# Kernel optimization log

Measured on AMD Instinct MI355X. Metric: run time of the kernel, lower is better.

## Reference

```python
import jax, jax.numpy as jnp
import numpy as np

N_NODES = 100000
N_EDGES = 3200000
N_GRAPHS = 64
NEG_SLOPE = 0.2


def mish(x):
    return x * jnp.tanh(jax.nn.softplus(x))


def gat_layer(x, src, dst, W, b, a_src, a_dst, heads, out_ch, n_nodes):
    # h: [N, H, C]
    h = (x @ W).reshape(n_nodes, heads, out_ch)
    alpha_s = jnp.sum(h * a_src[None], axis=-1)  # [N, H]
    alpha_d = jnp.sum(h * a_dst[None], axis=-1)  # [N, H]
    e = jax.nn.leaky_relu(alpha_s[src] + alpha_d[dst], NEG_SLOPE)  # [E, H]
    # scatter-softmax over incoming edges of each destination node
    emax = jax.ops.segment_max(e, dst, num_segments=n_nodes)  # [N, H]
    ee = jnp.exp(e - emax[dst])
    den = jax.ops.segment_sum(ee, dst, num_segments=n_nodes)
    alpha = ee / (den[dst] + 1e-16)  # [E, H]
    msg = h[src] * alpha[..., None]  # [E, H, C]
    out = jax.ops.segment_sum(msg, dst, num_segments=n_nodes)
    return out.reshape(n_nodes, heads * out_ch) + b


def setup_inputs() -> dict:
    key = jax.random.key(0)
    ks = jax.random.split(key, 10)
    x = jax.random.normal(ks[0], (N_NODES, 128), dtype=jnp.float32)
    edge_index = jax.random.randint(ks[1], (2, N_EDGES), 0, N_NODES, dtype=jnp.int64)
    batch = jnp.sort(jax.random.randint(ks[2], (N_NODES,), 0, N_GRAPHS, dtype=jnp.int64))
    s1 = 1.0 / np.sqrt(128.0)
    s2 = 1.0 / np.sqrt(16.0)
    return {
        "x": x,
        "edge_index": edge_index,
        "batch": batch,
        "W1": jax.random.normal(ks[3], (128, 16), dtype=jnp.float32) * s1,
        "b1": jnp.zeros((16,), dtype=jnp.float32),
        "a_src1": jax.random.normal(ks[4], (4, 4), dtype=jnp.float32) * 0.5,
        "a_dst1": jax.random.normal(ks[5], (4, 4), dtype=jnp.float32) * 0.5,
        "W2": jax.random.normal(ks[6], (16, 32), dtype=jnp.float32) * s2,
        "b2": jnp.zeros((32,), dtype=jnp.float32),
        "a_src2": jax.random.normal(ks[7], (1, 32), dtype=jnp.float32) * 0.5,
        "a_dst2": jax.random.normal(ks[8], (1, 32), dtype=jnp.float32) * 0.5,
    }


def reference(x, edge_index, batch, W1, b1, a_src1, a_dst1, W2, b2, a_src2, a_dst2):
    n = x.shape[0]
    # PyG GATConv default add_self_loops=True
    loop = jnp.arange(n, dtype=edge_index.dtype)
    src = jnp.concatenate([edge_index[0], loop])
    dst = jnp.concatenate([edge_index[1], loop])
    h = mish(gat_layer(x, src, dst, W1, b1, a_src1, a_dst1, heads=4, out_ch=4, n_nodes=n))
    h = mish(gat_layer(h, src, dst, W2, b2, a_src2, a_dst2, heads=1, out_ch=32, n_nodes=n))
    # global_mean_pool
    sums = jax.ops.segment_sum(h, batch, num_segments=N_GRAPHS)
    cnts = jax.ops.segment_sum(jnp.ones((n,), h.dtype), batch, num_segments=N_GRAPHS)
    return sums / jnp.maximum(cnts, 1.0)[:, None]
```

## Files before the change

kernel.cpp:

```cpp
#include <hip/hip_runtime.h>
#include <hip/hip_fp16.h>
#include <math.h>

#define NEG_SLOPE 0.2f
#define SB 512
#define NBMAX 2048
#define CAP 2816

typedef _Float16 half2v __attribute__((ext_vector_type(2)));
typedef _Float16 half4v __attribute__((ext_vector_type(4)));

__device__ __forceinline__ float mishf(float x) {
    if (x > 15.f) return x;
    float ex = __expf(x);
    float y = 1.f + ex;
    float y2 = y * y;
    return x * (y2 - 1.f) / (y2 + 1.f);
}

__device__ __forceinline__ float lw(float e) {
    return __expf(fmaxf(e, NEG_SLOPE * e));
}

__device__ __forceinline__ float hdot2a(half2v a, half2v b, float c) {
#if __has_builtin(__builtin_amdgcn_fdot2)
    return __builtin_amdgcn_fdot2(a, b, c, false);
#else
    return (float)a.x * (float)b.x + (float)a.y * (float)b.y + c;
#endif
}

__global__ void gemm1_kernel(const float* __restrict__ x, const float* __restrict__ W1,
                             const float* __restrict__ a_dst,
                             const float* __restrict__ W2, const float* __restrict__ as2,
                             const float* __restrict__ ad2,
                             _Float16* __restrict__ hpre1h, float* __restrict__ addst,
                             int* __restrict__ cursor, float* __restrict__ pool,
                             float* __restrict__ cnt, float* __restrict__ vs,
                             float* __restrict__ vd, int NB, int NG, int N) {
    __shared__ float Wlt[16 * 132];
    __shared__ float xs[16 * 132];
    int tid = threadIdx.x;
    if (blockIdx.x == 0) {
        for (int i = tid; i < NB; i += 256) cursor[i] = 0;
        for (int i = tid; i < NG * 32; i += 256) pool[i] = 0.f;
        for (int i = tid; i < NG; i += 256) cnt[i] = 0.f;
        if (tid < 16) {
            float ps = 0.f, pd = 0.f;
            #pragma unroll
            for (int c = 0; c < 32; c++) {
                float w = W2[tid * 32 + c];
                ps += w * as2[c];
                pd += w * ad2[c];
            }
            vs[tid] = ps; vd[tid] = pd;
        }
    }
    for (int i = tid; i < 2048; i += 256) Wlt[(i & 15) * 132 + (i >> 4)] = W1[i];
    int nodebase = blockIdx.x * 16;
    const float4* x4 = (const float4*)(x + (size_t)nodebase * 128);
    for (int i = tid; i < 512; i += 256) {
        float4 v = x4[i];
        int e = i * 4;
        int nl = e >> 7, k = e & 127;
        float* dp = &xs[nl * 132 + k];
        dp[0] = v.x; dp[1] = v.y; dp[2] = v.z; dp[3] = v.w;
    }
    __syncthreads();
    int nl = tid >> 4, ch = tid & 15;
    const float4* xr4 = (const float4*)&xs[nl * 132];
    const float4* wr4 = (const float4*)&Wlt[ch * 132];
    float acc = 0.f;
    #pragma unroll
    for (int k4 = 0; k4 < 32; k4++) {
        float4 xv = xr4[k4];
        float4 wv = wr4[k4];
        acc += xv.x * wv.x + xv.y * wv.y + xv.z * wv.z + xv.w * wv.w;
    }
    int node = nodebase + nl;
    if (node < N) {
        hpre1h[node * 16 + ch] = (_Float16)acc;
        float pd = acc * a_dst[ch];
        pd += __shfl_xor(pd, 1); pd += __shfl_xor(pd, 2);
        if ((ch & 3) == 0) addst[node * 4 + (ch >> 2)] = pd;
    }
}

__global__ __launch_bounds__(1024) void scatF_kernel(
        const int* __restrict__ src, const int* __restrict__ dst,
        int E, int Etot, int CH, int NB,
        int* __restrict__ cursor, int* __restrict__ pairs) {
    __shared__ int lcnt[NBMAX];
    __shared__ int lbase[NBMAX];
    int tid = threadIdx.x, blk = blockIdx.x;
    for (int b = tid; b < NB; b += 1024) lcnt[b] = 0;
    __syncthreads();
    int ibeg = blk * CH, iend = min((blk + 1) * CH, Etot);
    int cd[8];
    #pragma unroll
    for (int u = 0; u < 8; u++) {
        int i = ibeg + tid + (u << 10);
        int d = -1;
        if (i < iend) d = (i < E) ? dst[i] : (i - E);
        cd[u] = d;
        if (d >= 0) atomicAdd(&lcnt[d >> 6], 1);
    }
    for (int i = ibeg + (8 << 10) + tid; i < iend; i += 1024) {
        int d = (i < E) ? dst[i] : (i - E);
        atomicAdd(&lcnt[d >> 6], 1);
    }
    __syncthreads();
    for (int b = tid; b < NB; b += 1024) {
        int h = lcnt[b];
        lbase[b] = h ? atomicAdd(&cursor[b], h) : 0;
    }
    __syncthreads();
    for (int b = tid; b < NB; b += 1024) lcnt[b] = 0;
    __syncthreads();
    #pragma unroll
    for (int u = 0; u < 8; u++) {
        int i = ibeg + tid + (u << 10);
        int d = cd[u];
        if (d < 0) continue;
        int s = (i < E) ? src[i] : d;
        int b = d >> 6, dl = d & 63;
        int r = atomicAdd(&lcnt[b], 1);
        int pos = lbase[b] + r;
        pairs[(size_t)b * CAP + (pos < CAP ? pos : CAP - 1)] = s | (dl << 17);
    }
    for (int i = ibeg + (8 << 10) + tid; i < iend; i += 1024) {
        int d = (i < E) ? dst[i] : (i - E);
        int s = (i < E) ? src[i] : d;
        int b = d >> 6, dl = d & 63;
        int r = atomicAdd(&lcnt[b], 1);
        int pos = lbase[b] + r;
        pairs[(size_t)b * CAP + (pos < CAP ? pos : CAP - 1)] = s | (dl << 17);
    }
}

__global__ __launch_bounds__(256) void csragg1_kernel(
        const int* __restrict__ pairs, const int* __restrict__ btotal,
        int NB, int N,
        int* __restrict__ ssorted, int* __restrict__ rs, int* __restrict__ re,
        const float* __restrict__ a_src1, const float* __restrict__ addst,
        const _Float16* __restrict__ hpre1h, const float* __restrict__ b1,
        const float* __restrict__ vs, const float* __restrict__ vd,
        _Float16* __restrict__ hpost1h,
        float* __restrict__ as2n, float* __restrict__ ad2n) {
    __shared__ int deg[64];
    __shared__ int s[64];
    __shared__ int cur[64];
    __shared__ __attribute__((aligned(16))) int lds_sorted[CAP];
    int tid = threadIdx.x, b = blockIdx.x;
    int nb0 = b << 6;
    int cnt_nodes = min(64, N - nb0);
    int bstart = b * CAP;
    int total = min(btotal[b], CAP);
    int bend = bstart + total;
    if (tid < 64) deg[tid] = 0;
    __syncthreads();
    for (int j = bstart + tid; j < bend; j += 256)
        atomicAdd(&deg[(pairs[j] >> 17) & 63], 1);
    __syncthreads();
    if (tid < 64) s[tid] = deg[tid];
    __syncthreads();
    for (int o = 1; o < 64; o <<= 1) {
        int v = 0;
        if (tid < 64 && tid >= o) v = s[tid - o];
        __syncthreads();
        if (tid < 64) s[tid] += v;
        __syncthreads();
    }
    if (tid < 64) {
        int ex = s[tid] - deg[tid];
        cur[tid] = ex;
        if (tid < cnt_nodes) {
            rs[nb0 + tid] = bstart + ex;
            re[nb0 + tid] = bstart + ex + deg[tid];
        }
    }
    __syncthreads();
    for (int j = bstart + tid; j < bend; j += 256) {
        int p = pairs[j];
        int pos = atomicAdd(&cur[(p >> 17) & 63], 1);
        lds_sorted[pos] = p & 0x1FFFF;
    }
    __syncthreads();

    {
        int t4 = total >> 2;
        const int4* ls4 = (const int4*)lds_sorted;
        int4* gs4 = (int4*)(ssorted + bstart);
        for (int j = tid; j < t4; j += 256) gs4[j] = ls4[j];
        for (int j = (t4 << 2) + tid; j < total; j += 256)
            ssorted[bstart + j] = lds_sorted[j];
    }

    int wave = tid >> 6;
    int lane = tid & 63;
    int head = lane & 3, er = lane >> 2;
    int c0 = head * 4;
    half2v w01, w23;
    w01.x = (_Float16)a_src1[c0];     w01.y = (_Float16)a_src1[c0 + 1];
    w23.x = (_Float16)a_src1[c0 + 2]; w23.y = (_Float16)a_src1[c0 + 3];
    for (int r = 0; r < 16; r++) {
        int ln = (wave << 4) + r;
        if (ln >= cnt_nodes) break;
        int node = nb0 + ln;
        int end = cur[ln];
        int start = end - deg[ln];
        float adh = addst[node * 4 + head];
        float den = 0.f, a0 = 0.f, a1 = 0.f, a2 = 0.f, a3 = 0.f;
        int last = end - 1;
        int jb = start;
        for (; jb + 16 <= end; jb += 16) {
            int s0 = lds_sorted[jb + er];
            half4v h = *(const half4v*)(hpre1h + (size_t)s0 * 16 + c0);
            half2v hlo = __builtin_shufflevector(h, h, 0, 1);
            half2v hhi = __builtin_shufflevector(h, h, 2, 3);
            float p = hdot2a(hlo, w01, hdot2a(hhi, w23, 0.f));
            float w = lw(p + adh);
            den += w;
            a0 += (float)h.x * w; a1 += (float)h.y * w;
            a2 += (float)h.z * w; a3 += (float)h.w * w;
        }
        if (jb < end) {
            int j0 = jb + er;
            int k0 = (j0 <= last) ? j0 : last;
            int s0 = lds_sorted[k0];
            half4v h = *(const half4v*)(hpre1h + (size_t)s0 * 16 + c0);
            half2v hlo = __builtin_shufflevector(h, h, 0, 1);
            half2v hhi = __builtin_shufflevector(h, h, 2, 3);
            float p = hdot2a(hlo, w01, hdot2a(hhi, w23, 0.f));
            float w = (j0 <= last) ? lw(p + adh) : 0.f;
            den += w;
            a0 += (float)h.x * w; a1 += (float)h.y * w;
            a2 += (float)h.z * w; a3 += (float)h.w * w;
        }
        a0 += __shfl_xor(a0, 4);  a1 += __shfl_xor(a1, 4);  a2 += __shfl_xor(a2, 4);  a3 += __shfl_xor(a3, 4);  den += __shfl_xor(den, 4);
        a0 += __shfl_xor(a0, 8);  a1 += __shfl_xor(a1, 8);  a2 += __shfl_xor(a2, 8);  a3 += __shfl_xor(a3, 8);  den += __shfl_xor(den, 8);
        a0 += __shfl_xor(a0, 16); a1 += __shfl_xor(a1, 16); a2 += __shfl_xor(a2, 16); a3 += __shfl_xor(a3, 16); den += __shfl_xor(den, 16);
        a0 += __shfl_xor(a0, 32); a1 += __shfl_xor(a1, 32); a2 += __shfl_xor(a2, 32); a3 += __shfl_xor(a3, 32); den += __shfl_xor(den, 32);
        if (er == 0) {
            float inv = 1.f / (den + 1e-16f);
            float o0 = mishf(a0 * inv + b1[c0]);
            float o1 = mishf(a1 * inv + b1[c0 + 1]);
            float o2 = mishf(a2 * inv + b1[c0 + 2]);
            float o3 = mishf(a3 * inv + b1[c0 + 3]);
            half4v oh;
            oh.x = (_Float16)o0; oh.y = (_Float16)o1;
            oh.z = (_Float16)o2; oh.w = (_Float16)o3;
            *(half4v*)(hpost1h + (size_t)node * 16 + c0) = oh;
            float ps = o0 * vs[c0] + o1 * vs[c0 + 1] + o2 * vs[c0 + 2] + o3 * vs[c0 + 3];
            float pd = o0 * vd[c0] + o1 * vd[c0 + 1] + o2 * vd[c0 + 2] + o3 * vd[c0 + 3];
            ps += __shfl_xor(ps, 1); pd += __shfl_xor(pd, 1);
            ps += __shfl_xor(ps, 2); pd += __shfl_xor(pd, 2);
            if (head == 0) { as2n[node] = ps; ad2n[node] = pd; }
        }
    }
}

__global__ void agg2_kernel(const int* __restrict__ rs, const int* __restrict__ re,
                            const int* __restrict__ ssorted,
                            const float* __restrict__ as2n, const float* __restrict__ ad2n,
                            const _Float16* __restrict__ hpost1h,
                            float* __restrict__ agg16, float* __restrict__ denv, int N) {
    int wave = threadIdx.x >> 6;
    int lane = threadIdx.x & 63;
    int node = blockIdx.x * 4 + wave;
    if (node >= N) return;
    int start = rs[node], end = re[node];
    int q = lane & 3, er = lane >> 2;
    int c0 = q * 4;
    float adh = ad2n[node];
    const _Float16* hb = hpost1h + c0;
    float den = 0.f, a0 = 0.f, a1 = 0.f, a2 = 0.f, a3 = 0.f;
    int last = end - 1;
    int jb = start;
    for (; jb + 16 <= end; jb += 16) {
        int s0 = __builtin_nontemporal_load(ssorted + jb + er);
        float w = lw(as2n[s0] + adh);
        half4v h = *(const half4v*)(hb + (size_t)s0 * 16);
        den += w;
        a0 += (float)h.x * w; a1 += (float)h.y * w;
        a2 += (float)h.z * w; a3 += (float)h.w * w;
    }
    if (jb < end) {
        int j0 = jb + er;
        int k0 = (j0 <= last) ? j0 : last;
        int s0 = __builtin_nontemporal_load(ssorted + k0);
        float w = (j0 <= last) ? lw(as2n[s0] + adh) : 0.f;
        half4v h = *(const half4v*)(hb + (size_t)s0 * 16);
        den += w;
        a0 += (float)h.x * w; a1 += (float)h.y * w;
        a2 += (float)h.z * w; a3 += (float)h.w * w;
    }
    a0 += __shfl_xor(a0, 4);  a1 += __shfl_xor(a1, 4);  a2 += __shfl_xor(a2, 4);  a3 += __shfl_xor(a3, 4);  den += __shfl_xor(den, 4);
    a0 += __shfl_xor(a0, 8);  a1 += __shfl_xor(a1, 8);  a2 += __shfl_xor(a2, 8);  a3 += __shfl_xor(a3, 8);  den += __shfl_xor(den, 8);
    a0 += __shfl_xor(a0, 16); a1 += __shfl_xor(a1, 16); a2 += __shfl_xor(a2, 16); a3 += __shfl_xor(a3, 16); den += __shfl_xor(den, 16);
    a0 += __shfl_xor(a0, 32); a1 += __shfl_xor(a1, 32); a2 += __shfl_xor(a2, 32); a3 += __shfl_xor(a3, 32); den += __shfl_xor(den, 32);
    if (er == 0) {
        float4 o; o.x = a0; o.y = a1; o.z = a2; o.w = a3;
        *(float4*)(agg16 + (size_t)node * 16 + c0) = o;
        if (q == 0) denv[node] = den;
    }
}

__global__ void post2pool_kernel(const float* __restrict__ agg16, const float* __restrict__ denv,
                                 const float* __restrict__ W2, const float* __restrict__ b2,
                                 const int* __restrict__ batch,
                                 float* __restrict__ pool, float* __restrict__ cnt, int N) {
    __shared__ float Wl[16 * 32];
    int tid = threadIdx.x;
    for (int i = tid; i < 512; i += 256) Wl[i] = W2[i];
    __syncthreads();
    int r = tid >> 5, ch = tid & 31;
    float bc = b2[ch];
    int base = blockIdx.x * 512;
    int cur = -1;
    float sum = 0.f, c = 0.f;
    for (int it = 0; it < 64; it++) {
        int n = base + it * 8 + r;
        if (n >= N) break;
        int g = batch[n];
        if (g != cur) {
            if (cur >= 0) {
                atomicAdd(&pool[cur * 32 + ch], sum);
                if (ch == 0) atomicAdd(&cnt[cur], c);
            }
            cur = g; sum = 0.f; c = 0.f;
        }
        const float* ar = agg16 + (size_t)n * 16;
        float acc = 0.f;
        #pragma unroll
        for (int k = 0; k < 16; k++) acc += ar[k] * Wl[k * 32 + ch];
        float val = mishf(acc / (denv[n] + 1e-16f) + bc);
        sum += val;
        c += 1.f;
    }
    if (cur >= 0) {
        atomicAdd(&pool[cur * 32 + ch], sum);
        if (ch == 0) atomicAdd(&cnt[cur], c);
    }
}

__global__ void fin_kernel(const float* __restrict__ pool, const float* __restrict__ cnt,
                           float* __restrict__ out, int NG) {
    int i = blockIdx.x * blockDim.x + threadIdx.x;
    if (i >= NG * 32) return;
    out[i] = pool[i] / fmaxf(cnt[i >> 5], 1.0f);
}

extern "C" void kernel_launch(void* const* d_in, const int* in_sizes, int n_in,
                              void* d_out, int out_size, void* d_ws, size_t ws_size,
                              hipStream_t stream) {
    const float* x   = (const float*)d_in[0];
    const int* eidx  = (const int*)d_in[1];
    const int* batch = (const int*)d_in[2];
    const float* W1  = (const float*)d_in[3];
    const float* b1  = (const float*)d_in[4];
    const float* as1 = (const float*)d_in[5];
    const float* ad1 = (const float*)d_in[6];
    const float* W2  = (const float*)d_in[7];
    const float* b2  = (const float*)d_in[8];
    const float* as2 = (const float*)d_in[9];
    const float* ad2 = (const float*)d_in[10];
    float* out = (float*)d_out;

    int N = in_sizes[0] / 128;
    int E = in_sizes[1] / 2;
    int Etot = E + N;
    int NG = out_size / 32;
    const int* esrc = eidx;
    const int* edst = eidx + E;

    int NB = (N + 63) >> 6;
    int CH = (Etot + SB - 1) / SB;

    char* p = (char*)d_ws;
    auto alloc = [&](size_t nbytes) {
        p = (char*)(((uintptr_t)p + 15) & ~(uintptr_t)15);
        void* r = (void*)p; p += nbytes; return r;
    };
    int* pairs        = (int*)alloc((size_t)NB * CAP * 4);
    int* ssorted      = (int*)alloc((size_t)NB * CAP * 4);
    int* rs           = (int*)alloc((size_t)N * 4);
    int* re           = (int*)alloc((size_t)N * 4);
    int* cursor       = (int*)alloc((size_t)NB * 4);
    _Float16* hpre1h  = (_Float16*)alloc((size_t)N * 16 * 2);
    _Float16* hpost1h = (_Float16*)alloc((size_t)N * 16 * 2);
    float* addst1  = (float*)alloc((size_t)N * 4 * 4);
    float* as2n    = (float*)alloc((size_t)N * 4);
    float* ad2n    = (float*)alloc((size_t)N * 4);
    float* agg16   = (float*)alloc((size_t)N * 16 * 4);
    float* denv    = (float*)alloc((size_t)N * 4);
    float* vs      = (float*)alloc(16 * 4);
    float* vd      = (float*)alloc(16 * 4);
    float* pool    = (float*)alloc((size_t)NG * 32 * 4);
    float* cnt     = (float*)alloc((size_t)NG * 4);

    gemm1_kernel<<<(N + 15) / 16, 256, 0, stream>>>(x, W1, ad1, W2, as2, ad2,
                                                    hpre1h, addst1, cursor, pool, cnt,
                                                    vs, vd, NB, NG, N);
    scatF_kernel<<<SB, 1024, 0, stream>>>(esrc, edst, E, Etot, CH, NB, cursor, pairs);
    csragg1_kernel<<<NB, 256, 0, stream>>>(pairs, cursor, NB, N,
                                           ssorted, rs, re, as1, addst1, hpre1h,
                                           b1, vs, vd, hpost1h, as2n, ad2n);
    agg2_kernel<<<(N + 3) / 4, 256, 0, stream>>>(rs, re, ssorted, as2n, ad2n, hpost1h,
                                                 agg16, denv, N);
    post2pool_kernel<<<(N + 511) / 512, 256, 0, stream>>>(agg16, denv, W2, b2, batch,
                                                          pool, cnt, N);
    fin_kernel<<<(NG * 32 + 255) / 256, 256, 0, stream>>>(pool, cnt, out, NG);
}
```

Baseline: 336.1 us.

## Bucket edges by 128-node groups in scatter, split into halves in CSR build

```diff
diff --git a/kernel.cpp b/kernel.cpp
--- a/kernel.cpp
+++ b/kernel.cpp
@@ -3,9 +3,10 @@
 #include <math.h>
 
 #define NEG_SLOPE 0.2f
-#define SB 512
-#define NBMAX 2048
-#define CAP 2816
+#define SB 256
+#define NBMAX 1024
+#define CAP 5120
+#define CAPH 2816
 
 typedef _Float16 half2v __attribute__((ext_vector_type(2)));
 typedef _Float16 half4v __attribute__((ext_vector_type(4)));
@@ -96,18 +97,18 @@
     for (int b = tid; b < NB; b += 1024) lcnt[b] = 0;
     __syncthreads();
     int ibeg = blk * CH, iend = min((blk + 1) * CH, Etot);
-    int cd[8];
+    int cd[16];
     #pragma unroll
-    for (int u = 0; u < 8; u++) {
+    for (int u = 0; u < 16; u++) {
         int i = ibeg + tid + (u << 10);
         int d = -1;
         if (i < iend) d = (i < E) ? dst[i] : (i - E);
         cd[u] = d;
-        if (d >= 0) atomicAdd(&lcnt[d >> 6], 1);
-    }
-    for (int i = ibeg + (8 << 10) + tid; i < iend; i += 1024) {
+        if (d >= 0) atomicAdd(&lcnt[d >> 7], 1);
+    }
+    for (int i = ibeg + (16 << 10) + tid; i < iend; i += 1024) {
         int d = (i < E) ? dst[i] : (i - E);
-        atomicAdd(&lcnt[d >> 6], 1);
+        atomicAdd(&lcnt[d >> 7], 1);
     }
     __syncthreads();
     for (int b = tid; b < NB; b += 1024) {
@@ -118,20 +119,20 @@
     for (int b = tid; b < NB; b += 1024) lcnt[b] = 0;
     __syncthreads();
     #pragma unroll
-    for (int u = 0; u < 8; u++) {
+    for (int u = 0; u < 16; u++) {
         int i = ibeg + tid + (u << 10);
         int d = cd[u];
         if (d < 0) continue;
         int s = (i < E) ? src[i] : d;
-        int b = d >> 6, dl = d & 63;
+        int b = d >> 7, dl = d & 127;
         int r = atomicAdd(&lcnt[b], 1);
         int pos = lbase[b] + r;
         pairs[(size_t)b * CAP + (pos < CAP ? pos : CAP - 1)] = s | (dl << 17);
     }
-    for (int i = ibeg + (8 << 10) + tid; i < iend; i += 1024) {
+    for (int i = ibeg + (16 << 10) + tid; i < iend; i += 1024) {
         int d = (i < E) ? dst[i] : (i - E);
         int s = (i < E) ? src[i] : d;
-        int b = d >> 6, dl = d & 63;
+        int b = d >> 7, dl = d & 127;
         int r = atomicAdd(&lcnt[b], 1);
         int pos = lbase[b] + r;
         pairs[(size_t)b * CAP + (pos < CAP ? pos : CAP - 1)] = s | (dl << 17);
@@ -150,17 +151,26 @@
     __shared__ int deg[64];
     __shared__ int s[64];
     __shared__ int cur[64];
-    __shared__ __attribute__((aligned(16))) int lds_sorted[CAP];
-    int tid = threadIdx.x, b = blockIdx.x;
-    int nb0 = b << 6;
+    __shared__ int hcnt;
+    __shared__ __attribute__((aligned(16))) int lds_raw[CAPH];
+    __shared__ __attribute__((aligned(16))) int lds_sorted[CAPH];
+    int tid = threadIdx.x, bh = blockIdx.x;
+    int B = bh >> 1, half = bh & 1;
+    int nb0 = (B << 7) + (half << 6);
     int cnt_nodes = min(64, N - nb0);
-    int bstart = b * CAP;
-    int total = min(btotal[b], CAP);
-    int bend = bstart + total;
+    int bstart = B * CAP;
+    int total = min(btotal[B], CAP);
     if (tid < 64) deg[tid] = 0;
-    __syncthreads();
-    for (int j = bstart + tid; j < bend; j += 256)
-        atomicAdd(&deg[(pairs[j] >> 17) & 63], 1);
+    if (tid == 0) hcnt = 0;
+    __syncthreads();
+    for (int j = tid; j < total; j += 256) {
+        int p = pairs[bstart + j];
+        if (((p >> 23) & 1) == half) {
+            int r = atomicAdd(&hcnt, 1);
+            if (r < CAPH) lds_raw[r] = p;
+            atomicAdd(&deg[(p >> 17) & 63], 1);
+        }
+    }
     __syncthreads();
     if (tid < 64) s[tid] = deg[tid];
     __syncthreads();
@@ -175,25 +185,26 @@
         int ex = s[tid] - deg[tid];
         cur[tid] = ex;
         if (tid < cnt_nodes) {
-            rs[nb0 + tid] = bstart + ex;
-            re[nb0 + tid] = bstart + ex + deg[tid];
-        }
-    }
-    __syncthreads();
-    for (int j = bstart + tid; j < bend; j += 256) {
-        int p = pairs[j];
+            rs[nb0 + tid] = bh * CAPH + ex;
+            re[nb0 + tid] = bh * CAPH + ex + deg[tid];
+        }
+    }
+    __syncthreads();
+    int htot = min(hcnt, CAPH);
+    for (int j = tid; j < htot; j += 256) {
+        int p = lds_raw[j];
         int pos = atomicAdd(&cur[(p >> 17) & 63], 1);
-        lds_sorted[pos] = p & 0x1FFFF;
+        lds_sorted[pos < CAPH ? pos : CAPH - 1] = p & 0x1FFFF;
     }
     __syncthreads();
 
     {
-        int t4 = total >> 2;
+        int t4 = htot >> 2;
         const int4* ls4 = (const int4*)lds_sorted;
-        int4* gs4 = (int4*)(ssorted + bstart);
+        int4* gs4 = (int4*)(ssorted + (size_t)bh * CAPH);
         for (int j = tid; j < t4; j += 256) gs4[j] = ls4[j];
-        for (int j = (t4 << 2) + tid; j < total; j += 256)
-            ssorted[bstart + j] = lds_sorted[j];
+        for (int j = (t4 << 2) + tid; j < htot; j += 256)
+            ssorted[(size_t)bh * CAPH + j] = lds_sorted[j];
     }
 
     int wave = tid >> 6;
@@ -374,7 +385,8 @@
     const int* esrc = eidx;
     const int* edst = eidx + E;
 
-    int NB = (N + 63) >> 6;
+    int NB = (N + 127) >> 7;
+    int NBH = NB * 2;
     int CH = (Etot + SB - 1) / SB;
 
     char* p = (char*)d_ws;
@@ -383,7 +395,7 @@
         void* r = (void*)p; p += nbytes; return r;
     };
     int* pairs        = (int*)alloc((size_t)NB * CAP * 4);
-    int* ssorted      = (int*)alloc((size_t)NB * CAP * 4);
+    int* ssorted      = (int*)alloc((size_t)NBH * CAPH * 4);
     int* rs           = (int*)alloc((size_t)N * 4);
     int* re           = (int*)alloc((size_t)N * 4);
     int* cursor       = (int*)alloc((size_t)NB * 4);
@@ -403,9 +415,9 @@
                                                     hpre1h, addst1, cursor, pool, cnt,
                                                     vs, vd, NB, NG, N);
     scatF_kernel<<<SB, 1024, 0, stream>>>(esrc, edst, E, Etot, CH, NB, cursor, pairs);
-    csragg1_kernel<<<NB, 256, 0, stream>>>(pairs, cursor, NB, N,
-                                           ssorted, rs, re, as1, addst1, hpre1h,
-                                           b1, vs, vd, hpost1h, as2n, ad2n);
+    csragg1_kernel<<<NBH, 256, 0, stream>>>(pairs, cursor, NB, N,
+                                            ssorted, rs, re, as1, addst1, hpre1h,
+                                            b1, vs, vd, hpost1h, as2n, ad2n);
     agg2_kernel<<<(N + 3) / 4, 256, 0, stream>>>(rs, re, ssorted, as2n, ad2n, hpost1h,
                                                  agg16, denv, N);
     post2pool_kernel<<<(N + 511) / 512, 256, 0, stream>>>(agg16, denv, W2, b2, batch,
```

Result: slower. 351.4 us (+4.6%).
